# Performance work log

Hardware: AMD Instinct MI355X
Metric: run time of the kernel (lower is better)

## Reference

```python
import jax, jax.numpy as jnp
import numpy as np

COMMITMENT_COST = 0.25


def setup_inputs() -> dict:
    key = jax.random.key(0)
    k1, k2 = jax.random.split(key)
    inputs = jax.random.normal(k1, (32, 64, 64, 64), dtype=jnp.float32)  # (B, D, H, W)
    codewords = jax.random.uniform(k2, (512, 64), dtype=jnp.float32)    # (K, D)
    return {"inputs": inputs, "codewords": codewords}


def reference(inputs, codewords):
    # NCHW -> NHWC so last dim is codewords_dim
    x = jnp.transpose(inputs, (0, 2, 3, 1))          # (B, H, W, D)
    B, H, W, D = x.shape
    flat = x.reshape(-1, D)                          # (N, D)

    x_sq = jnp.sum(flat * flat, axis=1, keepdims=True)            # (N, 1)
    c_sq = jnp.sum(codewords * codewords, axis=1)[None, :]        # (1, K)
    dots = flat @ codewords.T                                     # (N, K)
    distances = x_sq + c_sq - 2.0 * dots                          # (N, K)

    encoding_indices = jnp.argmin(distances, axis=1)              # (N,)
    quantized = codewords[encoding_indices].reshape(B, H, W, D)   # (B, H, W, D)

    quantizing_loss = jnp.mean((jax.lax.stop_gradient(quantized) - x) ** 2)
    commitment_loss = jnp.mean((quantized - jax.lax.stop_gradient(x)) ** 2)
    loss = quantizing_loss + COMMITMENT_COST * commitment_loss

    # straight-through estimator
    quantized_st = x + jax.lax.stop_gradient(quantized - x)

    out = jnp.transpose(quantized_st, (0, 3, 1, 2))               # (B, D, H, W)
    return out, encoding_indices.reshape(B, H, W), loss
```

## Files before the change

### kernel.cpp

```cpp
#include <hip/hip_runtime.h>
#include <math.h>

#define HWSZ 4096
#define DIM  64
#define KCW  512
#define NROW 131072
#define CMAX 16
#define XP2  68
#define WVS  5056

typedef short bf16x8 __attribute__((ext_vector_type(8)));
typedef float f32x4  __attribute__((ext_vector_type(4)));

#define WS_CSQ  64
#define WS_BLOB 1024
#define WS_PART 17408

static __device__ __forceinline__ unsigned short f2bf(float f) {
    union { float f; unsigned u; } v; v.f = f;
    unsigned u = v.u;
    return (unsigned short)((u + 0x7fffu + ((u >> 16) & 1u)) >> 16);
}

__global__ void vq_prep_kernel(const float* __restrict__ cw, float* __restrict__ ws) {
    int tg = blockIdx.x * 256 + threadIdx.x;
    if (tg < KCW) {
        const float4* c4 = (const float4*)(cw + (size_t)tg * DIM);
        float s0 = 0.f, s1 = 0.f, s2 = 0.f, s3 = 0.f;
        #pragma unroll
        for (int i = 0; i < 16; ++i) {
            float4 c = c4[i];
            s0 = fmaf(c.x, c.x, s0); s1 = fmaf(c.y, c.y, s1);
            s2 = fmaf(c.z, c.z, s2); s3 = fmaf(c.w, c.w, s3);
        }
        ws[WS_CSQ + tg] = (s0 + s1) + (s2 + s3);
    }
    if (tg < 4096) {
        int l = tg & 63, f = (tg >> 6) & 1, kt = tg >> 7;
        int col = kt * 16 + (l & 15);
        unsigned short* blob = (unsigned short*)(ws + WS_BLOB);
        #pragma unroll
        for (int j = 0; j < 8; ++j) {
            int d = f * 32 + (l >> 4) * 8 + j;
            blob[((kt * 2 + f) * 64 + l) * 8 + j] = f2bf(cw[col * DIM + d]);
        }
    }
}

__global__ __attribute__((amdgpu_flat_work_group_size(256, 256), amdgpu_waves_per_eu(2, 2)))
void vq_main_kernel(const float* __restrict__ in, const float* __restrict__ cw,
                    const float* __restrict__ ws_ro, float* __restrict__ part,
                    float* __restrict__ out) {
    __shared__ float lds[4 * WVS];

    const int t  = threadIdx.x;
    const int w  = t >> 6, l = t & 63;
    const int hi = l >> 4, cl = l & 15;

    float* S     = lds + w * WVS;
    float* xw    = S;
    float* xsq   = S + 4352;
    int*   sidxp = (int*)(S + 4416);
    int*   cntsp = (int*)(S + 4480);
    unsigned short* candp = (unsigned short*)(S + 4544);

    const int b    = blockIdx.x >> 4;
    const int hwW  = (blockIdx.x & 15) * 256 + w * 64;
    const int rowW = blockIdx.x * 256 + w * 64;

    cntsp[l] = 0;

    const float* __restrict__ xg = in + (size_t)b * (DIM * HWSZ) + hwW;
    {
        const int tx = l & 15, dy = l >> 4;
        #pragma unroll
        for (int i = 0; i < 16; ++i) {
            int d = 4 * i + dy;
            *(float4*)(xw + d * XP2 + tx * 4) = *(const float4*)(xg + (size_t)d * HWSZ + tx * 4);
        }
    }

    {
        float s = 0.f;
        for (int d = 0; d < DIM; ++d) { float xv = xw[d * XP2 + l]; s = fmaf(xv, xv, s); }
        xsq[l] = s;
    }

    bf16x8 af[4][2];
    #pragma unroll
    for (int rgp = 0; rgp < 4; ++rgp)
        #pragma unroll
        for (int f = 0; f < 2; ++f)
            #pragma unroll
            for (int j = 0; j < 8; ++j)
                af[rgp][f][j] = (short)f2bf(-xw[(f * 32 + hi * 8 + j) * XP2 + rgp * 16 + cl]);

    const bf16x8* __restrict__ bp   = (const bf16x8*)(ws_ro + WS_BLOB);
    const float*  __restrict__ csqg = ws_ro + WS_CSQ;

    float mn[4][4];
    #pragma unroll
    for (int rgp = 0; rgp < 4; ++rgp)
        #pragma unroll
        for (int rg = 0; rg < 4; ++rg) mn[rgp][rg] = INFINITY;
    #pragma unroll 2
    for (int kt = 0; kt < 32; ++kt) {
        float ci = 0.5f * csqg[kt * 16 + cl];
        bf16x8 b0 = bp[(kt * 2 + 0) * 64 + l];
        bf16x8 b1 = bp[(kt * 2 + 1) * 64 + l];
        #pragma unroll
        for (int rgp = 0; rgp < 4; ++rgp) {
            f32x4 a = {ci, ci, ci, ci};
            a = __builtin_amdgcn_mfma_f32_16x16x32_bf16(af[rgp][0], b0, a, 0, 0, 0);
            a = __builtin_amdgcn_mfma_f32_16x16x32_bf16(af[rgp][1], b1, a, 0, 0, 0);
            #pragma unroll
            for (int rg = 0; rg < 4; ++rg) mn[rgp][rg] = fminf(mn[rgp][rg], a[rg]);
        }
    }
    #pragma unroll
    for (int off = 1; off < 16; off <<= 1)
        #pragma unroll
        for (int rgp = 0; rgp < 4; ++rgp)
            #pragma unroll
            for (int rg = 0; rg < 4; ++rg)
                mn[rgp][rg] = fminf(mn[rgp][rg], __shfl_xor(mn[rgp][rg], off, 64));

    float thr[4][4];
    #pragma unroll
    for (int rgp = 0; rgp < 4; ++rgp)
        #pragma unroll
        for (int rg = 0; rg < 4; ++rg)
            thr[rgp][rg] = mn[rgp][rg]
                         + 0.0625f * sqrtf(xsq[rgp * 16 + 4 * hi + rg]) + 0.03125f;

    #pragma unroll 2
    for (int kt = 0; kt < 32; ++kt) {
        float ci = 0.5f * csqg[kt * 16 + cl];
        bf16x8 b0 = bp[(kt * 2 + 0) * 64 + l];
        bf16x8 b1 = bp[(kt * 2 + 1) * 64 + l];
        #pragma unroll
        for (int rgp = 0; rgp < 4; ++rgp) {
            f32x4 a = {ci, ci, ci, ci};
            a = __builtin_amdgcn_mfma_f32_16x16x32_bf16(af[rgp][0], b0, a, 0, 0, 0);
            a = __builtin_amdgcn_mfma_f32_16x16x32_bf16(af[rgp][1], b1, a, 0, 0, 0);
            #pragma unroll
            for (int rg = 0; rg < 4; ++rg) {
                if (a[rg] <= thr[rgp][rg]) {
                    int r = rgp * 16 + 4 * hi + rg;
                    int pos = atomicAdd(&cntsp[r], 1);
                    if (pos < CMAX) candp[r * 16 + pos] = (unsigned short)(kt * 16 + cl);
                }
            }
        }
    }

    {
        const int r = l;
        const int n = cntsp[r];
        if (n <= CMAX) {
            float bb = INFINITY; int bkk = 0x7fffffff;
            const float xsqe = xsq[r];
            for (int s = 0; s < n; ++s) {
                int k = candp[r * 16 + s];
                const float4* __restrict__ c4 = (const float4*)(cw + (size_t)k * DIM);
                float d0 = 0.f, d1 = 0.f, d2 = 0.f, d3 = 0.f;
                #pragma unroll
                for (int i = 0; i < 16; ++i) {
                    float4 c = c4[i];
                    d0 = fmaf(xw[(4 * i + 0) * XP2 + r], c.x, d0);
                    d1 = fmaf(xw[(4 * i + 1) * XP2 + r], c.y, d1);
                    d2 = fmaf(xw[(4 * i + 2) * XP2 + r], c.z, d2);
                    d3 = fmaf(xw[(4 * i + 3) * XP2 + r], c.w, d3);
                }
                float dot  = (d0 + d1) + (d2 + d3);
                float dist = (xsqe + csqg[k]) - 2.f * dot;
                if (dist < bb || (dist == bb && k < bkk)) { bb = dist; bkk = k; }
            }
            sidxp[r] = bkk;
            out[(size_t)NROW * DIM + rowW + r] = (float)bkk;
        }
    }

    for (int r = 0; r < 64; ++r) {
        if (cntsp[r] <= CMAX) continue;
        const float xsqe = xsq[r];
        float bb = INFINITY; int bkk = 0x7fffffff;
        for (int kk = 0; kk < 8; ++kk) {
            int k = kk * 64 + l;
            const float4* __restrict__ c4 = (const float4*)(cw + (size_t)k * DIM);
            float d0 = 0.f, d1 = 0.f, d2 = 0.f, d3 = 0.f;
            #pragma unroll
            for (int i = 0; i < 16; ++i) {
                float4 c = c4[i];
                d0 = fmaf(xw[(4 * i + 0) * XP2 + r], c.x, d0);
                d1 = fmaf(xw[(4 * i + 1) * XP2 + r], c.y, d1);
                d2 = fmaf(xw[(4 * i + 2) * XP2 + r], c.z, d2);
                d3 = fmaf(xw[(4 * i + 3) * XP2 + r], c.w, d3);
            }
            float dot  = (d0 + d1) + (d2 + d3);
            float dist = (xsqe + csqg[k]) - 2.f * dot;
            if (dist < bb || (dist == bb && k < bkk)) { bb = dist; bkk = k; }
        }
        #pragma unroll
        for (int off = 32; off; off >>= 1) {
            float ob = __shfl_down(bb, off, 64);
            int   ok = __shfl_down(bkk, off, 64);
            if (ob < bb || (ob == bb && ok < bkk)) { bb = ob; bkk = ok; }
        }
        if (l == 0) {
            sidxp[r] = bkk;
            out[(size_t)NROW * DIM + rowW + r] = (float)bkk;
        }
    }

    {
        const int r = l;
        const int kwin = sidxp[r];
        const float4* __restrict__ qp = (const float4*)(cw + (size_t)kwin * DIM);
        float* __restrict__ obase = out + (size_t)b * (DIM * HWSZ) + hwW + r;
        float lsum = 0.f;
        #pragma unroll
        for (int dd = 0; dd < 16; ++dd) {
            float4 q4 = qp[dd];
            float qv[4] = {q4.x, q4.y, q4.z, q4.w};
            #pragma unroll
            for (int c = 0; c < 4; ++c) {
                int d = dd * 4 + c;
                float xv = xw[d * XP2 + r];
                obase[(size_t)d * HWSZ] = qv[c];
                float diff = qv[c] - xv;
                lsum = fmaf(diff, diff, lsum);
            }
        }
        #pragma unroll
        for (int off = 32; off; off >>= 1) lsum += __shfl_down(lsum, off, 64);
        if (l == 0) part[blockIdx.x * 4 + w] = lsum;
    }
}

__global__ void vq_finalize_kernel(const float* __restrict__ part, float* __restrict__ out) {
    __shared__ float wsum[4];
    const int t = threadIdx.x;
    float s = 0.f;
    #pragma unroll
    for (int i = 0; i < 8; ++i) s += part[t * 8 + i];
    #pragma unroll
    for (int off = 32; off; off >>= 1) s += __shfl_down(s, off, 64);
    if ((t & 63) == 0) wsum[t >> 6] = s;
    __syncthreads();
    if (t == 0)
        out[(size_t)NROW * DIM + NROW] =
            1.25f * ((wsum[0] + wsum[1]) + (wsum[2] + wsum[3])) / (float)((size_t)NROW * DIM);
}

extern "C" void kernel_launch(void* const* d_in, const int* in_sizes, int n_in,
                              void* d_out, int out_size, void* d_ws, size_t ws_size,
                              hipStream_t stream) {
    const float* in = (const float*)d_in[0];
    const float* cw = (const float*)d_in[1];
    float* out = (float*)d_out;
    float* ws  = (float*)d_ws;

    hipLaunchKernelGGL(vq_prep_kernel, dim3(16), dim3(256), 0, stream, cw, ws);
    hipLaunchKernelGGL(vq_main_kernel, dim3(NROW / 256), dim3(256), 0, stream,
                       in, cw, ws, ws + WS_PART, out);
    hipLaunchKernelGGL(vq_finalize_kernel, dim3(1), dim3(256), 0, stream, ws + WS_PART, out);
}
```

Baseline: 78.35 us.

## Drop LDS staging of input tile and read x from global to raise occupancy

Removes the per-wave LDS copy of the 64x64 input tile and reads x directly from global memory (relying on cache) for the norm, the bf16 fragment build, the rescoring and the loss. LDS use shrinks to small per-wave arrays, the waves-per-EU hint is widened to allow more resident waves, and the candidate list cap drops from 16 to 8. The trade-off is extra global/L2 reads of x, strided by HWSZ, across several phases. Rows overflowing the smaller cap also fall back more often to the full-codebook scan.

```diff
diff --git a/kernel.cpp b/kernel.cpp
--- a/kernel.cpp
+++ b/kernel.cpp
@@ -5,9 +5,7 @@
 #define DIM  64
 #define KCW  512
 #define NROW 131072
-#define CMAX 16
-#define XP2  68
-#define WVS  5056
+#define CMAX 8
 
 typedef short bf16x8 __attribute__((ext_vector_type(8)));
 typedef float f32x4  __attribute__((ext_vector_type(4)));
@@ -47,43 +45,32 @@
     }
 }
 
-__global__ __attribute__((amdgpu_flat_work_group_size(256, 256), amdgpu_waves_per_eu(2, 2)))
+__global__ __attribute__((amdgpu_flat_work_group_size(256, 256), amdgpu_waves_per_eu(2, 4)))
 void vq_main_kernel(const float* __restrict__ in, const float* __restrict__ cw,
                     const float* __restrict__ ws_ro, float* __restrict__ part,
                     float* __restrict__ out) {
-    __shared__ float lds[4 * WVS];
+    __shared__ float xsqa[4][64];
+    __shared__ int   sidxa[4][64];
+    __shared__ int   cntsa[4][64];
+    __shared__ int   canda[4][64][CMAX];
 
     const int t  = threadIdx.x;
     const int w  = t >> 6, l = t & 63;
     const int hi = l >> 4, cl = l & 15;
 
-    float* S     = lds + w * WVS;
-    float* xw    = S;
-    float* xsq   = S + 4352;
-    int*   sidxp = (int*)(S + 4416);
-    int*   cntsp = (int*)(S + 4480);
-    unsigned short* candp = (unsigned short*)(S + 4544);
-
     const int b    = blockIdx.x >> 4;
     const int hwW  = (blockIdx.x & 15) * 256 + w * 64;
     const int rowW = blockIdx.x * 256 + w * 64;
 
-    cntsp[l] = 0;
+    cntsa[w][l] = 0;
 
     const float* __restrict__ xg = in + (size_t)b * (DIM * HWSZ) + hwW;
-    {
-        const int tx = l & 15, dy = l >> 4;
-        #pragma unroll
-        for (int i = 0; i < 16; ++i) {
-            int d = 4 * i + dy;
-            *(float4*)(xw + d * XP2 + tx * 4) = *(const float4*)(xg + (size_t)d * HWSZ + tx * 4);
-        }
-    }
 
     {
         float s = 0.f;
-        for (int d = 0; d < DIM; ++d) { float xv = xw[d * XP2 + l]; s = fmaf(xv, xv, s); }
-        xsq[l] = s;
+        #pragma unroll
+        for (int d = 0; d < DIM; ++d) { float xv = xg[(size_t)d * HWSZ + l]; s = fmaf(xv, xv, s); }
+        xsqa[w][l] = s;
     }
 
     bf16x8 af[4][2];
@@ -93,7 +80,7 @@
         for (int f = 0; f < 2; ++f)
             #pragma unroll
             for (int j = 0; j < 8; ++j)
-                af[rgp][f][j] = (short)f2bf(-xw[(f * 32 + hi * 8 + j) * XP2 + rgp * 16 + cl]);
+                af[rgp][f][j] = (short)f2bf(-xg[(size_t)(f * 32 + hi * 8 + j) * HWSZ + rgp * 16 + cl]);
 
     const bf16x8* __restrict__ bp   = (const bf16x8*)(ws_ro + WS_BLOB);
     const float*  __restrict__ csqg = ws_ro + WS_CSQ;
@@ -131,7 +118,7 @@
         #pragma unroll
         for (int rg = 0; rg < 4; ++rg)
             thr[rgp][rg] = mn[rgp][rg]
-                         + 0.0625f * sqrtf(xsq[rgp * 16 + 4 * hi + rg]) + 0.03125f;
+                         + 0.0625f * sqrtf(xsqa[w][rgp * 16 + 4 * hi + rg]) + 0.03125f;
 
     #pragma unroll 2
     for (int kt = 0; kt < 32; ++kt) {
@@ -147,8 +134,8 @@
             for (int rg = 0; rg < 4; ++rg) {
                 if (a[rg] <= thr[rgp][rg]) {
                     int r = rgp * 16 + 4 * hi + rg;
-                    int pos = atomicAdd(&cntsp[r], 1);
-                    if (pos < CMAX) candp[r * 16 + pos] = (unsigned short)(kt * 16 + cl);
+                    int pos = atomicAdd(&cntsa[w][r], 1);
+                    if (pos < CMAX) canda[w][r][pos] = kt * 16 + cl;
                 }
             }
         }
@@ -156,34 +143,36 @@
 
     {
         const int r = l;
-        const int n = cntsp[r];
+        const int n = cntsa[w][r];
+        const float* __restrict__ xr = xg + r;
         if (n <= CMAX) {
             float bb = INFINITY; int bkk = 0x7fffffff;
-            const float xsqe = xsq[r];
+            const float xsqe = xsqa[w][r];
             for (int s = 0; s < n; ++s) {
-                int k = candp[r * 16 + s];
+                int k = canda[w][r][s];
                 const float4* __restrict__ c4 = (const float4*)(cw + (size_t)k * DIM);
                 float d0 = 0.f, d1 = 0.f, d2 = 0.f, d3 = 0.f;
                 #pragma unroll
                 for (int i = 0; i < 16; ++i) {
                     float4 c = c4[i];
-                    d0 = fmaf(xw[(4 * i + 0) * XP2 + r], c.x, d0);
-                    d1 = fmaf(xw[(4 * i + 1) * XP2 + r], c.y, d1);
-                    d2 = fmaf(xw[(4 * i + 2) * XP2 + r], c.z, d2);
-                    d3 = fmaf(xw[(4 * i + 3) * XP2 + r], c.w, d3);
+                    d0 = fmaf(xr[(size_t)(4 * i + 0) * HWSZ], c.x, d0);
+                    d1 = fmaf(xr[(size_t)(4 * i + 1) * HWSZ], c.y, d1);
+                    d2 = fmaf(xr[(size_t)(4 * i + 2) * HWSZ], c.z, d2);
+                    d3 = fmaf(xr[(size_t)(4 * i + 3) * HWSZ], c.w, d3);
                 }
                 float dot  = (d0 + d1) + (d2 + d3);
                 float dist = (xsqe + csqg[k]) - 2.f * dot;
                 if (dist < bb || (dist == bb && k < bkk)) { bb = dist; bkk = k; }
             }
-            sidxp[r] = bkk;
+            sidxa[w][r] = bkk;
             out[(size_t)NROW * DIM + rowW + r] = (float)bkk;
         }
     }
 
     for (int r = 0; r < 64; ++r) {
-        if (cntsp[r] <= CMAX) continue;
-        const float xsqe = xsq[r];
+        if (cntsa[w][r] <= CMAX) continue;
+        const float xsqe = xsqa[w][r];
+        const float* __restrict__ xr = xg + r;
         float bb = INFINITY; int bkk = 0x7fffffff;
         for (int kk = 0; kk < 8; ++kk) {
             int k = kk * 64 + l;
@@ -192,10 +181,10 @@
             #pragma unroll
             for (int i = 0; i < 16; ++i) {
                 float4 c = c4[i];
-                d0 = fmaf(xw[(4 * i + 0) * XP2 + r], c.x, d0);
-                d1 = fmaf(xw[(4 * i + 1) * XP2 + r], c.y, d1);
-                d2 = fmaf(xw[(4 * i + 2) * XP2 + r], c.z, d2);
-                d3 = fmaf(xw[(4 * i + 3) * XP2 + r], c.w, d3);
+                d0 = fmaf(xr[(size_t)(4 * i + 0) * HWSZ], c.x, d0);
+                d1 = fmaf(xr[(size_t)(4 * i + 1) * HWSZ], c.y, d1);
+                d2 = fmaf(xr[(size_t)(4 * i + 2) * HWSZ], c.z, d2);
+                d3 = fmaf(xr[(size_t)(4 * i + 3) * HWSZ], c.w, d3);
             }
             float dot  = (d0 + d1) + (d2 + d3);
             float dist = (xsqe + csqg[k]) - 2.f * dot;
@@ -208,15 +197,16 @@
             if (ob < bb || (ob == bb && ok < bkk)) { bb = ob; bkk = ok; }
         }
         if (l == 0) {
-            sidxp[r] = bkk;
+            sidxa[w][r] = bkk;
             out[(size_t)NROW * DIM + rowW + r] = (float)bkk;
         }
     }
 
     {
         const int r = l;
-        const int kwin = sidxp[r];
+        const int kwin = sidxa[w][r];
         const float4* __restrict__ qp = (const float4*)(cw + (size_t)kwin * DIM);
+        const float* __restrict__ xe = xg + r;
         float* __restrict__ obase = out + (size_t)b * (DIM * HWSZ) + hwW + r;
         float lsum = 0.f;
         #pragma unroll
@@ -226,7 +216,7 @@
             #pragma unroll
             for (int c = 0; c < 4; ++c) {
                 int d = dd * 4 + c;
-                float xv = xw[d * XP2 + r];
+                float xv = xe[(size_t)d * HWSZ];
                 obase[(size_t)d * HWSZ] = qv[c];
                 float diff = qv[c] - xv;
                 lsum = fmaf(diff, diff, lsum);
```

Measured after the change: 114.6 us. 1.46x slower.
